# Optimization experiments

Hardware: AMD Instinct MI355X
Metric: run time of the kernel (lower is better)

Reference implementation:

```python
import jax, jax.numpy as jnp
import numpy as np

N_NODES = 50000
N_EDGES = 800000
D = 64  # in_feat == hidden_channels


def _param(key, shape, fan_in):
    return jax.random.normal(key, shape, dtype=jnp.float32) / np.sqrt(fan_in)


def setup_inputs() -> dict:
    key = jax.random.key(0)
    ks = jax.random.split(key, 32)
    inp = {
        "x": jax.random.normal(ks[0], (N_NODES, D), dtype=jnp.float32),
        "edge_index": jax.random.randint(ks[1], (2, N_EDGES), 0, N_NODES, dtype=jnp.int64),
    }
    i = 2
    for l in (1, 2, 3):
        inp[f"W1_{l}"] = _param(ks[i + 0], (D, D), D)   # LEConv lin1 (source nodes)
        inp[f"b1_{l}"] = jnp.zeros((D,), jnp.float32)
        inp[f"W2_{l}"] = _param(ks[i + 1], (D, D), D)   # LEConv lin2 (target nodes, no bias)
        inp[f"W3_{l}"] = _param(ks[i + 2], (D, D), D)   # LEConv lin3 (root/self)
        inp[f"b3_{l}"] = jnp.zeros((D,), jnp.float32)
        inp[f"Wl_{l}"] = _param(ks[i + 3], (D, D), D)   # post-conv Linear
        inp[f"bl_{l}"] = jnp.zeros((D,), jnp.float32)
        i += 4
    return inp


def _leconv(x, src, dst, W1, b1, W2, W3, b3):
    # out_i = lin3(x_i) + sum_{j->i} (lin1(x_j) - lin2(x_i))
    a = x @ W1 + b1          # [N, D]
    b = x @ W2               # [N, D]
    msg = a[src] - b[dst]    # [E, D]  gather + elementwise
    agg = jax.ops.segment_sum(msg, dst, num_segments=x.shape[0])  # scatter-add
    return agg + (x @ W3 + b3)


def reference(x, edge_index,
              W1_1, b1_1, W2_1, W3_1, b3_1, Wl_1, bl_1,
              W1_2, b1_2, W2_2, W3_2, b3_2, Wl_2, bl_2,
              W1_3, b1_3, W2_3, W3_3, b3_3, Wl_3, bl_3):
    src, dst = edge_index[0], edge_index[1]
    h = x
    for (W1, b1, W2, W3, b3, Wl, bl) in (
        (W1_1, b1_1, W2_1, W3_1, b3_1, Wl_1, bl_1),
        (W1_2, b1_2, W2_2, W3_2, b3_2, Wl_2, bl_2),
        (W1_3, b1_3, W2_3, W3_3, b3_3, Wl_3, bl_3),
    ):
        h = _leconv(h, src, dst, W1, b1, W2, W3, b3)
        h = jax.nn.relu(h @ Wl + bl)
    return h
```

## Files before the change

kernel.cpp:

```cpp
#include <hip/hip_runtime.h>

#define N_NODES 50000
#define N_EDGES 800000
#define NCHUNK 64
#define NRANGE 4
#define RNODES (N_NODES / NRANGE)
#define CEDGES (N_EDGES / NCHUNK)
#define HIST_NB (NCHUNK * NRANGE)
#define SCAN_NB2 ((N_NODES + 63) / 64)

typedef __attribute__((ext_vector_type(8))) short short8;
typedef __attribute__((ext_vector_type(4))) float f32x4;

struct LPtrs { const float *W1, *W2, *W3, *Wl, *b1, *b3, *bl; };
struct AllPtrs { LPtrs l[3]; };

__device__ inline unsigned short f2b(float f) {
    union { float f; unsigned u; } c; c.f = f;
    return (unsigned short)((c.u + 0x7FFFu + ((c.u >> 16) & 1u)) >> 16);
}
__device__ inline float b2f(unsigned short h) {
    union { unsigned u; float f; } c; c.u = ((unsigned)h) << 16;
    return c.f;
}

__global__ __launch_bounds__(256) void histpack_kernel(const int* __restrict__ dst,
                                                       unsigned char* __restrict__ hist_part,
                                                       AllPtrs ap,
                                                       unsigned short* __restrict__ Wp,
                                                       float* __restrict__ rows) {
    __shared__ unsigned int h[5248];
    const int t = threadIdx.x;
    if (blockIdx.x < HIST_NB) {
        const int chunk = blockIdx.x >> 2;
        const int range = blockIdx.x & 3;
        const int nbase = range * RNODES;
        for (int i = t; i < RNODES / 4; i += 256) h[i] = 0u;
        __syncthreads();
        const int* dp = dst + chunk * CEDGES;
        for (int i = t; i < CEDGES; i += 256) {
            int d = dp[i] - nbase;
            if ((unsigned)d < (unsigned)RNODES)
                atomicAdd(&h[d >> 2], 1u << ((d & 3) * 8));
        }
        __syncthreads();
        unsigned int* out = (unsigned int*)(hist_part + (long)chunk * N_NODES + nbase);
        for (int i = t; i < RNODES / 4; i += 256) out[i] = h[i];
    } else {
        float* sW = (float*)h;
        float* sL = (float*)h + 64 * 65;
        const int wi = blockIdx.x - HIST_NB;
        const int layer = wi / 12;
        const int ct = wi % 12;
        LPtrs L = ap.l[layer];
        const float* Wm = (ct < 4) ? L.W1 : (ct < 8) ? L.W2 : L.W3;
        const int colb = (ct & 3) * 16;
        for (int i = t; i < 64 * 64; i += 256) sW[(i >> 6) * 65 + (i & 63)] = Wm[i];
        for (int i = t; i < 64 * 16; i += 256) {
            int q = i >> 4, c = i & 15;
            sL[q * 17 + c] = L.Wl[q * 64 + colb + c];
        }
        __syncthreads();
        for (int local = t; local < 1024; local += 256) {
            int j = local & 7, lane = (local >> 3) & 63, s = local >> 9;
            int k = s * 32 + (lane >> 4) * 8 + j;
            int c = lane & 15;
            float acc = 0.f;
            #pragma unroll 8
            for (int q = 0; q < 64; ++q) acc += sW[k * 65 + q] * sL[q * 17 + c];
            Wp[layer * 12288 + ct * 1024 + local] = f2b(acc);
        }
        if (ct == 0 && t < 64) {
            int col = t;
            float r1 = 0.f, r3 = 0.f;
            for (int q = 0; q < 64; ++q) {
                float wl = L.Wl[q * 64 + col];
                r1 += L.b1[q] * wl;
                r3 += L.b3[q] * wl;
            }
            rows[layer * 128 + col] = r1;
            rows[layer * 128 + 64 + col] = r3 + L.bl[col];
        }
    }
}

__global__ __launch_bounds__(256) void scanA2_kernel(unsigned char* __restrict__ hist_part,
                                                     int* __restrict__ off,
                                                     int* __restrict__ deg,
                                                     int* __restrict__ bsum) {
    __shared__ int part[4][64];
    const int t = threadIdx.x;
    const int ln = t & 63;
    const int cg = t >> 6;
    const int node = blockIdx.x * 64 + ln;
    unsigned char* col = hist_part + node;
    unsigned char v[16];
    int s = 0;
    if (node < N_NODES) {
        #pragma unroll
        for (int k = 0; k < 16; ++k) {
            v[k] = col[(long)(cg * 16 + k) * N_NODES];
            s += v[k];
        }
    }
    part[cg][ln] = s;
    __syncthreads();
    int run = 0, tot = 0;
    #pragma unroll
    for (int g = 0; g < 4; ++g) {
        int p = part[g][ln];
        if (g < cg) run += p;
        tot += p;
    }
    if (node < N_NODES) {
        #pragma unroll
        for (int k = 0; k < 16; ++k) {
            col[(long)(cg * 16 + k) * N_NODES] = (unsigned char)run;
            run += v[k];
        }
        if (cg == 0) deg[node] = tot;
    }
    if (cg == 0) {
        int x = tot;
        #pragma unroll
        for (int d = 1; d < 64; d <<= 1) {
            int u = __shfl_up(x, d, 64);
            if (ln >= d) x += u;
        }
        if (node < N_NODES) off[node] = x - tot;
        if (ln == 63) bsum[blockIdx.x] = x;
    }
}

__device__ __forceinline__ void gemm_body(int blk, int t,
    const unsigned short* __restrict__ hbf, const float* __restrict__ hf32,
    const unsigned short* __restrict__ Wp,
    const int* __restrict__ deg, const float* __restrict__ rows,
    unsigned short* __restrict__ abf, unsigned short* __restrict__ wbf, int n)
{
    const int lane = t & 63;
    const int quad = lane >> 4, lm = lane & 15;
    const int row_base = blk * 64 + (t >> 6) * 16;

    int arow = min(row_base + lm, n - 1);
    short8 a0, a1;
    if (hf32) {
        const float* hrow = hf32 + (long)arow * 64;
        #pragma unroll
        for (int j = 0; j < 8; ++j) {
            a0[j] = (short)f2b(hrow[quad * 8 + j]);
            a1[j] = (short)f2b(hrow[32 + quad * 8 + j]);
        }
    } else {
        const unsigned short* hrow = hbf + (long)arow * 64;
        a0 = *(const short8*)(hrow + quad * 8);
        a1 = *(const short8*)(hrow + 32 + quad * 8);
    }

    const short8* wp = (const short8*)Wp;
    f32x4 acc[12];
    #pragma unroll
    for (int ct = 0; ct < 12; ++ct) {
        f32x4 z = {0.f, 0.f, 0.f, 0.f};
        short8 w0 = wp[(ct * 2 + 0) * 64 + lane];
        short8 w1 = wp[(ct * 2 + 1) * 64 + lane];
        z = __builtin_amdgcn_mfma_f32_16x16x32_bf16(a0, w0, z, 0, 0, 0);
        z = __builtin_amdgcn_mfma_f32_16x16x32_bf16(a1, w1, z, 0, 0, 0);
        acc[ct] = z;
    }

    const int g0 = row_base + quad * 4;
    float dg[4];
    #pragma unroll
    for (int r = 0; r < 4; ++r) dg[r] = (float)deg[min(g0 + r, n - 1)];

    #pragma unroll
    for (int ct = 0; ct < 4; ++ct) {
        int col = ct * 16 + lm;
        float r1 = rows[col];
        float r3 = rows[64 + col];
        #pragma unroll
        for (int r = 0; r < 4; ++r) {
            int g = g0 + r;
            if (g < n) {
                abf[(long)g * 64 + col] = f2b(acc[ct][r]);
                float wv = acc[8 + ct][r] - dg[r] * (acc[4 + ct][r] - r1) + r3;
                wbf[(long)g * 64 + col] = f2b(wv);
            }
        }
    }
}

__global__ __launch_bounds__(256) void gemm3w_kernel(
    const unsigned short* __restrict__ hbf, const float* __restrict__ hf32,
    const unsigned short* __restrict__ Wp,
    const int* __restrict__ deg, const float* __restrict__ rows,
    unsigned short* __restrict__ abf, unsigned short* __restrict__ wbf, int n)
{
    gemm_body(blockIdx.x, threadIdx.x, hbf, hf32, Wp, deg, rows, abf, wbf, n);
}

__global__ __launch_bounds__(256) void fillgemm_kernel(
    const int* __restrict__ src, const int* __restrict__ dst,
    const int* __restrict__ off, const int* __restrict__ bsum,
    int* __restrict__ boff, const unsigned char* __restrict__ hist_part,
    int* __restrict__ csr,
    const float* __restrict__ x, const unsigned short* __restrict__ Wp,
    const int* __restrict__ deg, const float* __restrict__ rows,
    unsigned short* __restrict__ abf, unsigned short* __restrict__ wbf)
{
    __shared__ int cur[RNODES];
    __shared__ int sb[SCAN_NB2 + 2];
    if (blockIdx.x >= HIST_NB) {
        gemm_body(blockIdx.x - HIST_NB, threadIdx.x, nullptr, x, Wp, deg, rows,
                  abf, wbf, N_NODES);
        return;
    }
    const int t = threadIdx.x;

    int carry = 0;
    for (int base = 0; base < SCAN_NB2; base += 256) {
        int idx = base + t;
        int v = (idx < SCAN_NB2) ? bsum[idx] : 0;
        cur[t] = v;
        __syncthreads();
        #pragma unroll
        for (int d = 1; d < 256; d <<= 1) {
            int u = (t >= d) ? cur[t - d] : 0;
            __syncthreads();
            cur[t] += u;
            __syncthreads();
        }
        if (idx < SCAN_NB2) sb[idx] = carry + cur[t] - v;
        carry += cur[255];
        __syncthreads();
    }
    if (blockIdx.x == 0)
        for (int i = t; i < SCAN_NB2; i += 256) boff[i] = sb[i];

    const int chunk = blockIdx.x >> 2;
    const int range = blockIdx.x & 3;
    const int nbase = range * RNODES;
    const unsigned char* bp = hist_part + (long)chunk * N_NODES + nbase;
    const int* op = off + nbase;
    for (int i = t; i < RNODES; i += 256)
        cur[i] = op[i] + sb[(nbase + i) >> 6] + (int)bp[i];
    __syncthreads();
    const int* dp = dst + chunk * CEDGES;
    const int* sp = src + chunk * CEDGES;
    for (int i = t; i < CEDGES; i += 256) {
        int d = dp[i] - nbase;
        if ((unsigned)d < (unsigned)RNODES) {
            int pos = atomicAdd(&cur[d], 1);
            csr[pos] = sp[i];
        }
    }
}

__global__ __launch_bounds__(256) void gather_out_kernel(
    const int* __restrict__ off, const int* __restrict__ boff,
    const int* __restrict__ degv, const int* __restrict__ csr,
    const unsigned short* __restrict__ abf,
    const unsigned short* __restrict__ wbf,
    float* __restrict__ out_f, unsigned short* __restrict__ out_b, int last)
{
    int node = blockIdx.x * 4 + (threadIdx.x >> 6);
    int lane = threadIdx.x & 63;
    const int g = lane >> 4;
    const int f = (lane & 15) * 4;
    int beg = off[node] + boff[node >> 6];
    int end = beg + degv[node];
    float ax = 0.f, ay = 0.f, az = 0.f, aw = 0.f;
    int j = beg;
    for (; j + 16 <= end; j += 16) {
        int s0 = csr[j + g], s1 = csr[j + 4 + g];
        int s2 = csr[j + 8 + g], s3 = csr[j + 12 + g];
        ushort4 v0 = *(const ushort4*)(abf + (long)s0 * 64 + f);
        ushort4 v1 = *(const ushort4*)(abf + (long)s1 * 64 + f);
        ushort4 v2 = *(const ushort4*)(abf + (long)s2 * 64 + f);
        ushort4 v3 = *(const ushort4*)(abf + (long)s3 * 64 + f);
        ax += b2f(v0.x) + b2f(v1.x) + b2f(v2.x) + b2f(v3.x);
        ay += b2f(v0.y) + b2f(v1.y) + b2f(v2.y) + b2f(v3.y);
        az += b2f(v0.z) + b2f(v1.z) + b2f(v2.z) + b2f(v3.z);
        aw += b2f(v0.w) + b2f(v1.w) + b2f(v2.w) + b2f(v3.w);
    }
    for (; j + 8 <= end; j += 8) {
        int s0 = csr[j + g], s1 = csr[j + 4 + g];
        ushort4 v0 = *(const ushort4*)(abf + (long)s0 * 64 + f);
        ushort4 v1 = *(const ushort4*)(abf + (long)s1 * 64 + f);
        ax += b2f(v0.x) + b2f(v1.x);
        ay += b2f(v0.y) + b2f(v1.y);
        az += b2f(v0.z) + b2f(v1.z);
        aw += b2f(v0.w) + b2f(v1.w);
    }
    for (; j < end; j += 4) {
        int jj = j + g;
        if (jj < end) {
            int s0 = csr[jj];
            ushort4 v0 = *(const ushort4*)(abf + (long)s0 * 64 + f);
            ax += b2f(v0.x); ay += b2f(v0.y); az += b2f(v0.z); aw += b2f(v0.w);
        }
    }
    #pragma unroll
    for (int m = 16; m < 64; m <<= 1) {
        ax += __shfl_xor(ax, m, 64);
        ay += __shfl_xor(ay, m, 64);
        az += __shfl_xor(az, m, 64);
        aw += __shfl_xor(aw, m, 64);
    }
    if (g == 0) {
        ushort4 wv = *(const ushort4*)(wbf + (long)node * 64 + f);
        float o0 = fmaxf(ax + b2f(wv.x), 0.f);
        float o1 = fmaxf(ay + b2f(wv.y), 0.f);
        float o2 = fmaxf(az + b2f(wv.z), 0.f);
        float o3 = fmaxf(aw + b2f(wv.w), 0.f);
        if (last) {
            float4 o = {o0, o1, o2, o3};
            *(float4*)(out_f + (long)node * 64 + f) = o;
        } else {
            ushort4 o;
            o.x = f2b(o0); o.y = f2b(o1); o.z = f2b(o2); o.w = f2b(o3);
            *(ushort4*)(out_b + (long)node * 64 + f) = o;
        }
    }
}

extern "C" void kernel_launch(void* const* d_in, const int* in_sizes, int n_in,
                              void* d_out, int out_size, void* d_ws, size_t ws_size,
                              hipStream_t stream) {
    const float* x  = (const float*)d_in[0];
    const int*   ei = (const int*)d_in[1];
    const int*   src = ei;
    const int*   dst = ei + N_EDGES;

    char* wsb = (char*)d_ws;
    unsigned char*  hist_part = (unsigned char*)(wsb);
    unsigned short* abf  = (unsigned short*)(wsb + 12800000);
    unsigned short* wbf  = (unsigned short*)(wsb + 19200000);
    unsigned short* h1   = (unsigned short*)(wsb + 25600000);
    unsigned short* Wp   = (unsigned short*)(wsb + 38400000);
    float*          rows = (float*)(wsb + 38500000);
    int* off  = (int*)(wsb + 38600000);
    int* deg  = off + N_NODES;
    int* bsum = deg + N_NODES;
    int* boff = bsum + 1024;
    int* csr  = boff + 1024;

    const int NBLK = (N_NODES + 63) / 64;

    AllPtrs ap;
    for (int l = 0; l < 3; ++l) {
        int base = 2 + l * 7;
        ap.l[l].W1 = (const float*)d_in[base + 0];
        ap.l[l].b1 = (const float*)d_in[base + 1];
        ap.l[l].W2 = (const float*)d_in[base + 2];
        ap.l[l].W3 = (const float*)d_in[base + 3];
        ap.l[l].b3 = (const float*)d_in[base + 4];
        ap.l[l].Wl = (const float*)d_in[base + 5];
        ap.l[l].bl = (const float*)d_in[base + 6];
    }

    histpack_kernel<<<HIST_NB + 36, 256, 0, stream>>>(dst, hist_part, ap, Wp, rows);
    scanA2_kernel<<<SCAN_NB2, 256, 0, stream>>>(hist_part, off, deg, bsum);
    fillgemm_kernel<<<HIST_NB + NBLK, 256, 0, stream>>>(
        src, dst, off, bsum, boff, hist_part, csr,
        x, Wp, deg, rows, abf, wbf);

    gather_out_kernel<<<N_NODES / 4, 256, 0, stream>>>(
        off, boff, deg, csr, abf, wbf, (float*)d_out, h1, 0);

    const unsigned short* hin = h1;
    for (int l = 1; l < 3; ++l) {
        gemm3w_kernel<<<NBLK, 256, 0, stream>>>(
            hin, nullptr, Wp + l * 12288, deg, rows + l * 128,
            abf, wbf, N_NODES);
        gather_out_kernel<<<N_NODES / 4, 256, 0, stream>>>(
            off, boff, deg, csr, abf, wbf, (float*)d_out, h1, (l == 2));
        hin = h1;
    }
}
```

Measured before the change: 266.8 us.

## Split CSR histogram/fill into eight node ranges and single-pass block-sum scan

Doubles the number of node ranges per edge chunk (8 instead of 4) with a padded node count, so histogram and CSR-fill blocks use smaller shared arrays and more blocks run in parallel. The block-sum scan in the fill kernel is replaced by a single 256-thread scan over 4-element groups, removing the multi-pass loop. The cost is that each block now rereads its full edge chunk, so dst reads double. It also adds padding bytes to the histogram buffer, which must be sized for N_PAD.

```diff
diff --git a/kernel.cpp b/kernel.cpp
--- a/kernel.cpp
+++ b/kernel.cpp
@@ -1,13 +1,14 @@
 #include <hip/hip_runtime.h>
 
 #define N_NODES 50000
+#define N_PAD 50048
 #define N_EDGES 800000
 #define NCHUNK 64
-#define NRANGE 4
-#define RNODES (N_NODES / NRANGE)
+#define NRANGE 8
+#define RN 6256
 #define CEDGES (N_EDGES / NCHUNK)
 #define HIST_NB (NCHUNK * NRANGE)
-#define SCAN_NB2 ((N_NODES + 63) / 64)
+#define SCAN_NB2 (N_PAD / 64)
 
 typedef __attribute__((ext_vector_type(8))) short short8;
 typedef __attribute__((ext_vector_type(4))) float f32x4;
@@ -32,20 +33,20 @@
     __shared__ unsigned int h[5248];
     const int t = threadIdx.x;
     if (blockIdx.x < HIST_NB) {
-        const int chunk = blockIdx.x >> 2;
-        const int range = blockIdx.x & 3;
-        const int nbase = range * RNODES;
-        for (int i = t; i < RNODES / 4; i += 256) h[i] = 0u;
+        const int chunk = blockIdx.x >> 3;
+        const int range = blockIdx.x & 7;
+        const int nbase = range * RN;
+        for (int i = t; i < RN / 4; i += 256) h[i] = 0u;
         __syncthreads();
         const int* dp = dst + chunk * CEDGES;
         for (int i = t; i < CEDGES; i += 256) {
             int d = dp[i] - nbase;
-            if ((unsigned)d < (unsigned)RNODES)
+            if ((unsigned)d < (unsigned)RN)
                 atomicAdd(&h[d >> 2], 1u << ((d & 3) * 8));
         }
         __syncthreads();
-        unsigned int* out = (unsigned int*)(hist_part + (long)chunk * N_NODES + nbase);
-        for (int i = t; i < RNODES / 4; i += 256) out[i] = h[i];
+        unsigned int* out = (unsigned int*)(hist_part + (long)chunk * N_PAD + nbase);
+        for (int i = t; i < RN / 4; i += 256) out[i] = h[i];
     } else {
         float* sW = (float*)h;
         float* sL = (float*)h + 64 * 65;
@@ -96,12 +97,10 @@
     unsigned char* col = hist_part + node;
     unsigned char v[16];
     int s = 0;
-    if (node < N_NODES) {
-        #pragma unroll
-        for (int k = 0; k < 16; ++k) {
-            v[k] = col[(long)(cg * 16 + k) * N_NODES];
-            s += v[k];
-        }
+    #pragma unroll
+    for (int k = 0; k < 16; ++k) {
+        v[k] = col[(long)(cg * 16 + k) * N_PAD];
+        s += v[k];
     }
     part[cg][ln] = s;
     __syncthreads();
@@ -112,14 +111,12 @@
         if (g < cg) run += p;
         tot += p;
     }
-    if (node < N_NODES) {
-        #pragma unroll
-        for (int k = 0; k < 16; ++k) {
-            col[(long)(cg * 16 + k) * N_NODES] = (unsigned char)run;
-            run += v[k];
-        }
-        if (cg == 0) deg[node] = tot;
-    }
+    #pragma unroll
+    for (int k = 0; k < 16; ++k) {
+        col[(long)(cg * 16 + k) * N_PAD] = (unsigned char)run;
+        run += v[k];
+    }
+    if (cg == 0 && node < N_NODES) deg[node] = tot;
     if (cg == 0) {
         int x = tot;
         #pragma unroll
@@ -209,8 +206,8 @@
     const int* __restrict__ deg, const float* __restrict__ rows,
     unsigned short* __restrict__ abf, unsigned short* __restrict__ wbf)
 {
-    __shared__ int cur[RNODES];
-    __shared__ int sb[SCAN_NB2 + 2];
+    __shared__ int cur[RN];
+    __shared__ int sb[1024];
     if (blockIdx.x >= HIST_NB) {
         gemm_body(blockIdx.x - HIST_NB, threadIdx.x, nullptr, x, Wp, deg, rows,
                   abf, wbf, N_NODES);
@@ -218,39 +215,44 @@
     }
     const int t = threadIdx.x;
 
-    int carry = 0;
-    for (int base = 0; base < SCAN_NB2; base += 256) {
-        int idx = base + t;
-        int v = (idx < SCAN_NB2) ? bsum[idx] : 0;
-        cur[t] = v;
-        __syncthreads();
-        #pragma unroll
-        for (int d = 1; d < 256; d <<= 1) {
-            int u = (t >= d) ? cur[t - d] : 0;
-            __syncthreads();
-            cur[t] += u;
-            __syncthreads();
-        }
-        if (idx < SCAN_NB2) sb[idx] = carry + cur[t] - v;
-        carry += cur[255];
-        __syncthreads();
-    }
+    const int i0 = t * 4;
+    int a0 = (i0 + 0 < SCAN_NB2) ? bsum[i0 + 0] : 0;
+    int a1 = (i0 + 1 < SCAN_NB2) ? bsum[i0 + 1] : 0;
+    int a2 = (i0 + 2 < SCAN_NB2) ? bsum[i0 + 2] : 0;
+    int a3 = (i0 + 3 < SCAN_NB2) ? bsum[i0 + 3] : 0;
+    int s = a0 + a1 + a2 + a3;
+    cur[t] = s;
+    __syncthreads();
+    #pragma unroll
+    for (int d = 1; d < 256; d <<= 1) {
+        int u = (t >= d) ? cur[t - d] : 0;
+        __syncthreads();
+        cur[t] += u;
+        __syncthreads();
+    }
+    int excl = cur[t] - s;
+    sb[i0 + 0] = excl;
+    sb[i0 + 1] = excl + a0;
+    sb[i0 + 2] = excl + a0 + a1;
+    sb[i0 + 3] = excl + a0 + a1 + a2;
+    __syncthreads();
     if (blockIdx.x == 0)
         for (int i = t; i < SCAN_NB2; i += 256) boff[i] = sb[i];
 
-    const int chunk = blockIdx.x >> 2;
-    const int range = blockIdx.x & 3;
-    const int nbase = range * RNODES;
-    const unsigned char* bp = hist_part + (long)chunk * N_NODES + nbase;
+    const int chunk = blockIdx.x >> 3;
+    const int range = blockIdx.x & 7;
+    const int nbase = range * RN;
+    const unsigned char* bp = hist_part + (long)chunk * N_PAD + nbase;
     const int* op = off + nbase;
-    for (int i = t; i < RNODES; i += 256)
+    const int lim = min(RN, N_NODES - nbase);
+    for (int i = t; i < lim; i += 256)
         cur[i] = op[i] + sb[(nbase + i) >> 6] + (int)bp[i];
     __syncthreads();
     const int* dp = dst + chunk * CEDGES;
     const int* sp = src + chunk * CEDGES;
     for (int i = t; i < CEDGES; i += 256) {
         int d = dp[i] - nbase;
-        if ((unsigned)d < (unsigned)RNODES) {
+        if ((unsigned)d < (unsigned)RN) {
             int pos = atomicAdd(&cur[d], 1);
             csr[pos] = sp[i];
         }
```

Result: no change. 262.7 us (-1.5%).

## Replace chunked byte-histogram CSR build with global atomic degree count and fill

Applied to the files above, without the earlier changes.

Replaces the per-chunk shared-memory byte-histogram, the column scan and the chunked fill with a simpler pipeline: zero deg, count degrees with global atomics, run a single-block 1024-thread scan over padded nodes, then fill the CSR through global atomic cursors. This removes the 12.8 MB hist_part buffer and its strided traffic. In exchange it adds one more launch, a serial single-block scan, and global atomic contention. The CSR order within a node becomes nondeterministic, which can change summation order.

```diff
diff --git a/kernel.cpp b/kernel.cpp
--- a/kernel.cpp
+++ b/kernel.cpp
@@ -1,13 +1,10 @@
 #include <hip/hip_runtime.h>
 
 #define N_NODES 50000
+#define N_PAD 50176
 #define N_EDGES 800000
-#define NCHUNK 64
-#define NRANGE 4
-#define RNODES (N_NODES / NRANGE)
-#define CEDGES (N_EDGES / NCHUNK)
-#define HIST_NB (NCHUNK * NRANGE)
-#define SCAN_NB2 ((N_NODES + 63) / 64)
+#define FILLB 1024
+#define ZB 196
 
 typedef __attribute__((ext_vector_type(8))) short short8;
 typedef __attribute__((ext_vector_type(4))) float f32x4;
@@ -24,32 +21,18 @@
     return c.f;
 }
 
-__global__ __launch_bounds__(256) void histpack_kernel(const int* __restrict__ dst,
-                                                       unsigned char* __restrict__ hist_part,
+__global__ __launch_bounds__(256) void zeropack_kernel(int* __restrict__ deg,
                                                        AllPtrs ap,
                                                        unsigned short* __restrict__ Wp,
                                                        float* __restrict__ rows) {
-    __shared__ unsigned int h[5248];
+    __shared__ float sbuf[5248];
     const int t = threadIdx.x;
-    if (blockIdx.x < HIST_NB) {
-        const int chunk = blockIdx.x >> 2;
-        const int range = blockIdx.x & 3;
-        const int nbase = range * RNODES;
-        for (int i = t; i < RNODES / 4; i += 256) h[i] = 0u;
-        __syncthreads();
-        const int* dp = dst + chunk * CEDGES;
-        for (int i = t; i < CEDGES; i += 256) {
-            int d = dp[i] - nbase;
-            if ((unsigned)d < (unsigned)RNODES)
-                atomicAdd(&h[d >> 2], 1u << ((d & 3) * 8));
-        }
-        __syncthreads();
-        unsigned int* out = (unsigned int*)(hist_part + (long)chunk * N_NODES + nbase);
-        for (int i = t; i < RNODES / 4; i += 256) out[i] = h[i];
+    if (blockIdx.x < ZB) {
+        deg[blockIdx.x * 256 + t] = 0;
     } else {
-        float* sW = (float*)h;
-        float* sL = (float*)h + 64 * 65;
-        const int wi = blockIdx.x - HIST_NB;
+        float* sW = sbuf;
+        float* sL = sbuf + 64 * 65;
+        const int wi = blockIdx.x - ZB;
         const int layer = wi / 12;
         const int ct = wi % 12;
         LPtrs L = ap.l[layer];
@@ -84,51 +67,44 @@
     }
 }
 
-__global__ __launch_bounds__(256) void scanA2_kernel(unsigned char* __restrict__ hist_part,
-                                                     int* __restrict__ off,
-                                                     int* __restrict__ deg,
-                                                     int* __restrict__ bsum) {
-    __shared__ int part[4][64];
+__global__ __launch_bounds__(256) void deg_kernel(const int* __restrict__ dst,
+                                                  int* __restrict__ deg) {
+    int i = blockIdx.x * 256 + threadIdx.x;
+    atomicAdd(&deg[dst[i]], 1);
+}
+
+__global__ __launch_bounds__(1024) void scan_kernel(const int* __restrict__ deg,
+                                                    int* __restrict__ rowbeg,
+                                                    int* __restrict__ gcur) {
+    __shared__ int ws[16];
     const int t = threadIdx.x;
-    const int ln = t & 63;
-    const int cg = t >> 6;
-    const int node = blockIdx.x * 64 + ln;
-    unsigned char* col = hist_part + node;
-    unsigned char v[16];
+    const int base = t * 49;
     int s = 0;
-    if (node < N_NODES) {
+    for (int k = 0; k < 49; ++k) s += deg[base + k];
+    int x = s;
+    #pragma unroll
+    for (int d = 1; d < 64; d <<= 1) {
+        int u = __shfl_up(x, d, 64);
+        if ((t & 63) >= d) x += u;
+    }
+    if ((t & 63) == 63) ws[t >> 6] = x;
+    __syncthreads();
+    if (t < 16) {
+        int y = ws[t];
         #pragma unroll
-        for (int k = 0; k < 16; ++k) {
-            v[k] = col[(long)(cg * 16 + k) * N_NODES];
-            s += v[k];
-        }
-    }
-    part[cg][ln] = s;
+        for (int d = 1; d < 16; d <<= 1) {
+            int u = __shfl_up(y, d, 16);
+            if (t >= d) y += u;
+        }
+        ws[t] = y;
+    }
     __syncthreads();
-    int run = 0, tot = 0;
-    #pragma unroll
-    for (int g = 0; g < 4; ++g) {
-        int p = part[g][ln];
-        if (g < cg) run += p;
-        tot += p;
-    }
-    if (node < N_NODES) {
-        #pragma unroll
-        for (int k = 0; k < 16; ++k) {
-            col[(long)(cg * 16 + k) * N_NODES] = (unsigned char)run;
-            run += v[k];
-        }
-        if (cg == 0) deg[node] = tot;
-    }
-    if (cg == 0) {
-        int x = tot;
-        #pragma unroll
-        for (int d = 1; d < 64; d <<= 1) {
-            int u = __shfl_up(x, d, 64);
-            if (ln >= d) x += u;
-        }
-        if (node < N_NODES) off[node] = x - tot;
-        if (ln == 63) bsum[blockIdx.x] = x;
+    int run = ((t >> 6) ? ws[(t >> 6) - 1] : 0) + x - s;
+    for (int k = 0; k < 49; ++k) {
+        int i = base + k;
+        rowbeg[i] = run;
+        gcur[i] = run;
+        run += deg[i];
     }
 }
 
@@ -202,64 +178,27 @@
 
 __global__ __launch_bounds__(256) void fillgemm_kernel(
     const int* __restrict__ src, const int* __restrict__ dst,
-    const int* __restrict__ off, const int* __restrict__ bsum,
-    int* __restrict__ boff, const unsigned char* __restrict__ hist_part,
-    int* __restrict__ csr,
+    int* __restrict__ gcur, int* __restrict__ csr,
     const float* __restrict__ x, const unsigned short* __restrict__ Wp,
     const int* __restrict__ deg, const float* __restrict__ rows,
     unsigned short* __restrict__ abf, unsigned short* __restrict__ wbf)
 {
-    __shared__ int cur[RNODES];
-    __shared__ int sb[SCAN_NB2 + 2];
-    if (blockIdx.x >= HIST_NB) {
-        gemm_body(blockIdx.x - HIST_NB, threadIdx.x, nullptr, x, Wp, deg, rows,
+    if (blockIdx.x >= FILLB) {
+        gemm_body(blockIdx.x - FILLB, threadIdx.x, nullptr, x, Wp, deg, rows,
                   abf, wbf, N_NODES);
         return;
     }
-    const int t = threadIdx.x;
-
-    int carry = 0;
-    for (int base = 0; base < SCAN_NB2; base += 256) {
-        int idx = base + t;
-        int v = (idx < SCAN_NB2) ? bsum[idx] : 0;
-        cur[t] = v;
-        __syncthreads();
-        #pragma unroll
-        for (int d = 1; d < 256; d <<= 1) {
-            int u = (t >= d) ? cur[t - d] : 0;
-            __syncthreads();
-            cur[t] += u;
-            __syncthreads();
-        }
-        if (idx < SCAN_NB2) sb[idx] = carry + cur[t] - v;
-        carry += cur[255];
-        __syncthreads();
-    }
-    if (blockIdx.x == 0)
-        for (int i = t; i < SCAN_NB2; i += 256) boff[i] = sb[i];
-
-    const int chunk = blockIdx.x >> 2;
-    const int range = blockIdx.x & 3;
-    const int nbase = range * RNODES;
-    const unsigned char* bp = hist_part + (long)chunk * N_NODES + nbase;
-    const int* op = off + nbase;
-    for (int i = t; i < RNODES; i += 256)
-        cur[i] = op[i] + sb[(nbase + i) >> 6] + (int)bp[i];
-    __syncthreads();
-    const int* dp = dst + chunk * CEDGES;
-    const int* sp = src + chunk * CEDGES;
-    for (int i = t; i < CEDGES; i += 256) {
-        int d = dp[i] - nbase;
-        if ((unsigned)d < (unsigned)RNODES) {
-            int pos = atomicAdd(&cur[d], 1);
-            csr[pos] = sp[i];
-        }
+    for (int i = blockIdx.x * 256 + threadIdx.x; i < N_EDGES; i += FILLB * 256) {
+        int d = dst[i];
+        int s = src[i];
+        int pos = atomicAdd(&gcur[d], 1);
+        csr[pos] = s;
     }
 }
 
 __global__ __launch_bounds__(256) void gather_out_kernel(
-    const int* __restrict__ off, const int* __restrict__ boff,
-    const int* __restrict__ degv, const int* __restrict__ csr,
+    const int* __restrict__ rowbeg, const int* __restrict__ degv,
+    const int* __restrict__ csr,
     const unsigned short* __restrict__ abf,
     const unsigned short* __restrict__ wbf,
     float* __restrict__ out_f, unsigned short* __restrict__ out_b, int last)
@@ -268,7 +207,7 @@
     int lane = threadIdx.x & 63;
     const int g = lane >> 4;
     const int f = (lane & 15) * 4;
-    int beg = off[node] + boff[node >> 6];
+    int beg = rowbeg[node];
     int end = beg + degv[node];
     float ax = 0.f, ay = 0.f, az = 0.f, aw = 0.f;
     int j = beg;
@@ -334,17 +273,15 @@
     const int*   dst = ei + N_EDGES;
 
     char* wsb = (char*)d_ws;
-    unsigned char*  hist_part = (unsigned char*)(wsb);
-    unsigned short* abf  = (unsigned short*)(wsb + 12800000);
-    unsigned short* wbf  = (unsigned short*)(wsb + 19200000);
-    unsigned short* h1   = (unsigned short*)(wsb + 25600000);
-    unsigned short* Wp   = (unsigned short*)(wsb + 38400000);
-    float*          rows = (float*)(wsb + 38500000);
-    int* off  = (int*)(wsb + 38600000);
-    int* deg  = off + N_NODES;
-    int* bsum = deg + N_NODES;
-    int* boff = bsum + 1024;
-    int* csr  = boff + 1024;
+    unsigned short* abf  = (unsigned short*)(wsb);
+    unsigned short* wbf  = (unsigned short*)(wsb + 6400000);
+    unsigned short* h1   = (unsigned short*)(wsb + 12800000);
+    unsigned short* Wp   = (unsigned short*)(wsb + 19200000);
+    float*          rows = (float*)(wsb + 19300000);
+    int* deg    = (int*)(wsb + 19400000);
+    int* rowbeg = deg + N_PAD;
+    int* gcur   = rowbeg + N_PAD;
+    int* csr    = gcur + N_PAD;
 
     const int NBLK = (N_NODES + 63) / 64;
 
@@ -360,14 +297,14 @@
         ap.l[l].bl = (const float*)d_in[base + 6];
     }
 
-    histpack_kernel<<<HIST_NB + 36, 256, 0, stream>>>(dst, hist_part, ap, Wp, rows);
-    scanA2_kernel<<<SCAN_NB2, 256, 0, stream>>>(hist_part, off, deg, bsum);
-    fillgemm_kernel<<<HIST_NB + NBLK, 256, 0, stream>>>(
-        src, dst, off, bsum, boff, hist_part, csr,
-        x, Wp, deg, rows, abf, wbf);
+    zeropack_kernel<<<ZB + 36, 256, 0, stream>>>(deg, ap, Wp, rows);
+    deg_kernel<<<N_EDGES / 256, 256, 0, stream>>>(dst, deg);
+    scan_kernel<<<1, 1024, 0, stream>>>(deg, rowbeg, gcur);
+    fillgemm_kernel<<<FILLB + NBLK, 256, 0, stream>>>(
+        src, dst, gcur, csr, x, Wp, deg, rows, abf, wbf);
 
     gather_out_kernel<<<N_NODES / 4, 256, 0, stream>>>(
-        off, boff, deg, csr, abf, wbf, (float*)d_out, h1, 0);
+        rowbeg, deg, csr, abf, wbf, (float*)d_out, h1, 0);
 
     const unsigned short* hin = h1;
     for (int l = 1; l < 3; ++l) {
@@ -375,7 +312,7 @@
             hin, nullptr, Wp + l * 12288, deg, rows + l * 128,
             abf, wbf, N_NODES);
         gather_out_kernel<<<N_NODES / 4, 256, 0, stream>>>(
-            off, boff, deg, csr, abf, wbf, (float*)d_out, h1, (l == 2));
+            rowbeg, deg, csr, abf, wbf, (float*)d_out, h1, (l == 2));
         hin = h1;
     }
 }
```

New measurement: 351.9 us. +31.9%, slower.

## Aggregate raw bf16 features before projection and overlap next-layer GEMM with gather

Applied to the files above, without the earlier changes.

By linearity, the source-side projection is applied after neighbour aggregation. The gather sums raw bf16 node features into S, and a new out_kernel does S·(W1·Wl) plus the precomputed self/target term and ReLU. The self/target GEMM is folded into the gather grid as extra blocks, so it runs alongside the gather, and the x-to-bf16 cast moves into the histogram kernel. The histogram uses 128 chunks over a padded node range, with a simpler single-pass block scan. The aim is to drop the per-layer abf write and the standalone GEMM launches, at the cost of an extra small GEMM kernel per layer and an extra S round trip.

```diff
diff --git a/kernel.cpp b/kernel.cpp
--- a/kernel.cpp
+++ b/kernel.cpp
@@ -1,13 +1,16 @@
 #include <hip/hip_runtime.h>
 
 #define N_NODES 50000
+#define N_PAD 50176
 #define N_EDGES 800000
-#define NCHUNK 64
+#define NCHUNK 128
 #define NRANGE 4
-#define RNODES (N_NODES / NRANGE)
+#define RNODES 12544
 #define CEDGES (N_EDGES / NCHUNK)
 #define HIST_NB (NCHUNK * NRANGE)
-#define SCAN_NB2 ((N_NODES + 63) / 64)
+#define SCAN_NB 782
+#define GATB 12500
+#define NBLK 782
 
 typedef __attribute__((ext_vector_type(8))) short short8;
 typedef __attribute__((ext_vector_type(4))) float f32x4;
@@ -24,11 +27,11 @@
     return c.f;
 }
 
-__global__ __launch_bounds__(256) void histpack_kernel(const int* __restrict__ dst,
-                                                       unsigned char* __restrict__ hist_part,
-                                                       AllPtrs ap,
-                                                       unsigned short* __restrict__ Wp,
-                                                       float* __restrict__ rows) {
+__global__ __launch_bounds__(256) void histcast_kernel(
+    const int* __restrict__ dst, unsigned char* __restrict__ hist_part,
+    AllPtrs ap, unsigned short* __restrict__ Wp, float* __restrict__ rows,
+    const float* __restrict__ x, unsigned short* __restrict__ h0)
+{
     __shared__ unsigned int h[5248];
     const int t = threadIdx.x;
     if (blockIdx.x < HIST_NB) {
@@ -44,9 +47,9 @@
                 atomicAdd(&h[d >> 2], 1u << ((d & 3) * 8));
         }
         __syncthreads();
-        unsigned int* out = (unsigned int*)(hist_part + (long)chunk * N_NODES + nbase);
+        unsigned int* out = (unsigned int*)(hist_part + (long)chunk * N_PAD + nbase);
         for (int i = t; i < RNODES / 4; i += 256) out[i] = h[i];
-    } else {
+    } else if (blockIdx.x < HIST_NB + 36) {
         float* sW = (float*)h;
         float* sL = (float*)h + 64 * 65;
         const int wi = blockIdx.x - HIST_NB;
@@ -81,6 +84,24 @@
             rows[layer * 128 + col] = r1;
             rows[layer * 128 + 64 + col] = r3 + L.bl[col];
         }
+    } else {
+        const int cb = blockIdx.x - HIST_NB - 36;
+        const long base = (long)cb * 4096 + t * 16;
+        if (base < (long)N_NODES * 64) {
+            const float4* xp = (const float4*)(x + base);
+            float4 f0 = xp[0], f1 = xp[1], f2 = xp[2], f3 = xp[3];
+            short8 r0, r1v;
+            r0[0] = (short)f2b(f0.x); r0[1] = (short)f2b(f0.y);
+            r0[2] = (short)f2b(f0.z); r0[3] = (short)f2b(f0.w);
+            r0[4] = (short)f2b(f1.x); r0[5] = (short)f2b(f1.y);
+            r0[6] = (short)f2b(f1.z); r0[7] = (short)f2b(f1.w);
+            r1v[0] = (short)f2b(f2.x); r1v[1] = (short)f2b(f2.y);
+            r1v[2] = (short)f2b(f2.z); r1v[3] = (short)f2b(f2.w);
+            r1v[4] = (short)f2b(f3.x); r1v[5] = (short)f2b(f3.y);
+            r1v[6] = (short)f2b(f3.z); r1v[7] = (short)f2b(f3.w);
+            *(short8*)(h0 + base) = r0;
+            *(short8*)(h0 + base + 8) = r1v;
+        }
     }
 }
 
@@ -94,14 +115,12 @@
     const int cg = t >> 6;
     const int node = blockIdx.x * 64 + ln;
     unsigned char* col = hist_part + node;
-    unsigned char v[16];
+    unsigned char v[32];
     int s = 0;
-    if (node < N_NODES) {
-        #pragma unroll
-        for (int k = 0; k < 16; ++k) {
-            v[k] = col[(long)(cg * 16 + k) * N_NODES];
-            s += v[k];
-        }
+    #pragma unroll
+    for (int k = 0; k < 32; ++k) {
+        v[k] = col[(long)(cg * 32 + k) * N_PAD];
+        s += v[k];
     }
     part[cg][ln] = s;
     __syncthreads();
@@ -112,58 +131,46 @@
         if (g < cg) run += p;
         tot += p;
     }
-    if (node < N_NODES) {
-        #pragma unroll
-        for (int k = 0; k < 16; ++k) {
-            col[(long)(cg * 16 + k) * N_NODES] = (unsigned char)run;
-            run += v[k];
-        }
-        if (cg == 0) deg[node] = tot;
+    #pragma unroll
+    for (int k = 0; k < 32; ++k) {
+        col[(long)(cg * 32 + k) * N_PAD] = (unsigned char)run;
+        run += v[k];
     }
     if (cg == 0) {
-        int x = tot;
+        deg[node] = tot;
+        int xv = tot;
         #pragma unroll
         for (int d = 1; d < 64; d <<= 1) {
-            int u = __shfl_up(x, d, 64);
-            if (ln >= d) x += u;
-        }
-        if (node < N_NODES) off[node] = x - tot;
-        if (ln == 63) bsum[blockIdx.x] = x;
-    }
-}
-
-__device__ __forceinline__ void gemm_body(int blk, int t,
-    const unsigned short* __restrict__ hbf, const float* __restrict__ hf32,
-    const unsigned short* __restrict__ Wp,
+            int u = __shfl_up(xv, d, 64);
+            if (ln >= d) xv += u;
+        }
+        off[node] = xv - tot;
+        if (ln == 63) bsum[blockIdx.x] = xv;
+    }
+}
+
+__device__ __forceinline__ void gemmw_body(int blk, int t,
+    const unsigned short* __restrict__ hbf, const unsigned short* __restrict__ Wp,
     const int* __restrict__ deg, const float* __restrict__ rows,
-    unsigned short* __restrict__ abf, unsigned short* __restrict__ wbf, int n)
+    unsigned short* __restrict__ wbf, int n)
 {
     const int lane = t & 63;
     const int quad = lane >> 4, lm = lane & 15;
     const int row_base = blk * 64 + (t >> 6) * 16;
 
     int arow = min(row_base + lm, n - 1);
-    short8 a0, a1;
-    if (hf32) {
-        const float* hrow = hf32 + (long)arow * 64;
-        #pragma unroll
-        for (int j = 0; j < 8; ++j) {
-            a0[j] = (short)f2b(hrow[quad * 8 + j]);
-            a1[j] = (short)f2b(hrow[32 + quad * 8 + j]);
-        }
-    } else {
-        const unsigned short* hrow = hbf + (long)arow * 64;
-        a0 = *(const short8*)(hrow + quad * 8);
-        a1 = *(const short8*)(hrow + 32 + quad * 8);
-    }
+    const unsigned short* hrow = hbf + (long)arow * 64;
+    short8 a0 = *(const short8*)(hrow + quad * 8);
+    short8 a1 = *(const short8*)(hrow + 32 + quad * 8);
 
     const short8* wp = (const short8*)Wp;
-    f32x4 acc[12];
-    #pragma unroll
-    for (int ct = 0; ct < 12; ++ct) {
+    f32x4 acc[8];
+    #pragma unroll
+    for (int ct = 0; ct < 8; ++ct) {
+        int tile = ct + 4;
         f32x4 z = {0.f, 0.f, 0.f, 0.f};
-        short8 w0 = wp[(ct * 2 + 0) * 64 + lane];
-        short8 w1 = wp[(ct * 2 + 1) * 64 + lane];
+        short8 w0 = wp[(tile * 2 + 0) * 64 + lane];
+        short8 w1 = wp[(tile * 2 + 1) * 64 + lane];
         z = __builtin_amdgcn_mfma_f32_16x16x32_bf16(a0, w0, z, 0, 0, 0);
         z = __builtin_amdgcn_mfma_f32_16x16x32_bf16(a1, w1, z, 0, 0, 0);
         acc[ct] = z;
@@ -183,67 +190,62 @@
         for (int r = 0; r < 4; ++r) {
             int g = g0 + r;
             if (g < n) {
-                abf[(long)g * 64 + col] = f2b(acc[ct][r]);
-                float wv = acc[8 + ct][r] - dg[r] * (acc[4 + ct][r] - r1) + r3;
+                float wv = acc[4 + ct][r] - dg[r] * (acc[ct][r] - r1) + r3;
                 wbf[(long)g * 64 + col] = f2b(wv);
             }
         }
     }
 }
 
-__global__ __launch_bounds__(256) void gemm3w_kernel(
-    const unsigned short* __restrict__ hbf, const float* __restrict__ hf32,
-    const unsigned short* __restrict__ Wp,
-    const int* __restrict__ deg, const float* __restrict__ rows,
-    unsigned short* __restrict__ abf, unsigned short* __restrict__ wbf, int n)
-{
-    gemm_body(blockIdx.x, threadIdx.x, hbf, hf32, Wp, deg, rows, abf, wbf, n);
-}
-
-__global__ __launch_bounds__(256) void fillgemm_kernel(
+__global__ __launch_bounds__(256) void fillw_kernel(
     const int* __restrict__ src, const int* __restrict__ dst,
     const int* __restrict__ off, const int* __restrict__ bsum,
     int* __restrict__ boff, const unsigned char* __restrict__ hist_part,
     int* __restrict__ csr,
-    const float* __restrict__ x, const unsigned short* __restrict__ Wp,
+    const unsigned short* __restrict__ h0, const unsigned short* __restrict__ Wp,
     const int* __restrict__ deg, const float* __restrict__ rows,
-    unsigned short* __restrict__ abf, unsigned short* __restrict__ wbf)
+    unsigned short* __restrict__ wbf)
 {
     __shared__ int cur[RNODES];
-    __shared__ int sb[SCAN_NB2 + 2];
+    __shared__ int sb[1024];
     if (blockIdx.x >= HIST_NB) {
-        gemm_body(blockIdx.x - HIST_NB, threadIdx.x, nullptr, x, Wp, deg, rows,
-                  abf, wbf, N_NODES);
+        gemmw_body(blockIdx.x - HIST_NB, threadIdx.x, h0, Wp, deg, rows,
+                   wbf, N_NODES);
         return;
     }
     const int t = threadIdx.x;
 
-    int carry = 0;
-    for (int base = 0; base < SCAN_NB2; base += 256) {
-        int idx = base + t;
-        int v = (idx < SCAN_NB2) ? bsum[idx] : 0;
-        cur[t] = v;
+    const int i0 = t * 4;
+    int a0 = (i0 + 0 < SCAN_NB) ? bsum[i0 + 0] : 0;
+    int a1 = (i0 + 1 < SCAN_NB) ? bsum[i0 + 1] : 0;
+    int a2 = (i0 + 2 < SCAN_NB) ? bsum[i0 + 2] : 0;
+    int a3 = (i0 + 3 < SCAN_NB) ? bsum[i0 + 3] : 0;
+    int s = a0 + a1 + a2 + a3;
+    cur[t] = s;
+    __syncthreads();
+    #pragma unroll
+    for (int d = 1; d < 256; d <<= 1) {
+        int u = (t >= d) ? cur[t - d] : 0;
         __syncthreads();
-        #pragma unroll
-        for (int d = 1; d < 256; d <<= 1) {
-            int u = (t >= d) ? cur[t - d] : 0;
-            __syncthreads();
-            cur[t] += u;
-            __syncthreads();
-        }
-        if (idx < SCAN_NB2) sb[idx] = carry + cur[t] - v;
-        carry += cur[255];
+        cur[t] += u;
         __syncthreads();
     }
+    int excl = cur[t] - s;
+    sb[i0 + 0] = excl;
+    sb[i0 + 1] = excl + a0;
+    sb[i0 + 2] = excl + a0 + a1;
+    sb[i0 + 3] = excl + a0 + a1 + a2;
+    __syncthreads();
     if (blockIdx.x == 0)
-        for (int i = t; i < SCAN_NB2; i += 256) boff[i] = sb[i];
+        for (int i = t; i < SCAN_NB; i += 256) boff[i] = sb[i];
 
     const int chunk = blockIdx.x >> 2;
     const int range = blockIdx.x & 3;
     const int nbase = range * RNODES;
-    const unsigned char* bp = hist_part + (long)chunk * N_NODES + nbase;
+    const unsigned char* bp = hist_part + (long)chunk * N_PAD + nbase;
     const int* op = off + nbase;
-    for (int i = t; i < RNODES; i += 256)
+    const int lim = min(RNODES, N_NODES - nbase);
+    for (int i = t; i < lim; i += 256)
         cur[i] = op[i] + sb[(nbase + i) >> 6] + (int)bp[i];
     __syncthreads();
     const int* dp = dst + chunk * CEDGES;
@@ -257,13 +259,18 @@
     }
 }
 
-__global__ __launch_bounds__(256) void gather_out_kernel(
+__global__ __launch_bounds__(256) void gatherw_kernel(
     const int* __restrict__ off, const int* __restrict__ boff,
     const int* __restrict__ degv, const int* __restrict__ csr,
-    const unsigned short* __restrict__ abf,
-    const unsigned short* __restrict__ wbf,
-    float* __restrict__ out_f, unsigned short* __restrict__ out_b, int last)
+    const unsigned short* __restrict__ hbf, unsigned short* __restrict__ Sbf,
+    const unsigned short* __restrict__ Wp, const float* __restrict__ rows,
+    unsigned short* __restrict__ wbf)
 {
+    if (blockIdx.x >= GATB) {
+        gemmw_body(blockIdx.x - GATB, threadIdx.x, hbf, Wp, degv, rows,
+                   wbf, N_NODES);
+        return;
+    }
     int node = blockIdx.x * 4 + (threadIdx.x >> 6);
     int lane = threadIdx.x & 63;
     const int g = lane >> 4;
@@ -275,10 +282,10 @@
     for (; j + 16 <= end; j += 16) {
         int s0 = csr[j + g], s1 = csr[j + 4 + g];
         int s2 = csr[j + 8 + g], s3 = csr[j + 12 + g];
-        ushort4 v0 = *(const ushort4*)(abf + (long)s0 * 64 + f);
-        ushort4 v1 = *(const ushort4*)(abf + (long)s1 * 64 + f);
-        ushort4 v2 = *(const ushort4*)(abf + (long)s2 * 64 + f);
-        ushort4 v3 = *(const ushort4*)(abf + (long)s3 * 64 + f);
+        ushort4 v0 = *(const ushort4*)(hbf + (long)s0 * 64 + f);
+        ushort4 v1 = *(const ushort4*)(hbf + (long)s1 * 64 + f);
+        ushort4 v2 = *(const ushort4*)(hbf + (long)s2 * 64 + f);
+        ushort4 v3 = *(const ushort4*)(hbf + (long)s3 * 64 + f);
         ax += b2f(v0.x) + b2f(v1.x) + b2f(v2.x) + b2f(v3.x);
         ay += b2f(v0.y) + b2f(v1.y) + b2f(v2.y) + b2f(v3.y);
         az += b2f(v0.z) + b2f(v1.z) + b2f(v2.z) + b2f(v3.z);
@@ -286,8 +293,8 @@
     }
     for (; j + 8 <= end; j += 8) {
         int s0 = csr[j + g], s1 = csr[j + 4 + g];
-        ushort4 v0 = *(const ushort4*)(abf + (long)s0 * 64 + f);
-        ushort4 v1 = *(const ushort4*)(abf + (long)s1 * 64 + f);
+        ushort4 v0 = *(const ushort4*)(hbf + (long)s0 * 64 + f);
+        ushort4 v1 = *(const ushort4*)(hbf + (long)s1 * 64 + f);
         ax += b2f(v0.x) + b2f(v1.x);
         ay += b2f(v0.y) + b2f(v1.y);
         az += b2f(v0.z) + b2f(v1.z);
@@ -297,7 +304,7 @@
         int jj = j + g;
         if (jj < end) {
             int s0 = csr[jj];
-            ushort4 v0 = *(const ushort4*)(abf + (long)s0 * 64 + f);
+            ushort4 v0 = *(const ushort4*)(hbf + (long)s0 * 64 + f);
             ax += b2f(v0.x); ay += b2f(v0.y); az += b2f(v0.z); aw += b2f(v0.w);
         }
     }
@@ -309,18 +316,52 @@
         aw += __shfl_xor(aw, m, 64);
     }
     if (g == 0) {
-        ushort4 wv = *(const ushort4*)(wbf + (long)node * 64 + f);
-        float o0 = fmaxf(ax + b2f(wv.x), 0.f);
-        float o1 = fmaxf(ay + b2f(wv.y), 0.f);
-        float o2 = fmaxf(az + b2f(wv.z), 0.f);
-        float o3 = fmaxf(aw + b2f(wv.w), 0.f);
-        if (last) {
-            float4 o = {o0, o1, o2, o3};
-            *(float4*)(out_f + (long)node * 64 + f) = o;
-        } else {
-            ushort4 o;
-            o.x = f2b(o0); o.y = f2b(o1); o.z = f2b(o2); o.w = f2b(o3);
-            *(ushort4*)(out_b + (long)node * 64 + f) = o;
+        ushort4 o;
+        o.x = f2b(ax); o.y = f2b(ay); o.z = f2b(az); o.w = f2b(aw);
+        *(ushort4*)(Sbf + (long)node * 64 + f) = o;
+    }
+}
+
+__global__ __launch_bounds__(256) void out_kernel(
+    const unsigned short* __restrict__ Sbf, const unsigned short* __restrict__ wbf,
+    const unsigned short* __restrict__ Wp,
+    unsigned short* __restrict__ hout, float* __restrict__ fout, int last, int n)
+{
+    const int t = threadIdx.x;
+    const int lane = t & 63;
+    const int quad = lane >> 4, lm = lane & 15;
+    const int row_base = blockIdx.x * 64 + (t >> 6) * 16;
+
+    int arow = min(row_base + lm, n - 1);
+    const unsigned short* srow = Sbf + (long)arow * 64;
+    short8 a0 = *(const short8*)(srow + quad * 8);
+    short8 a1 = *(const short8*)(srow + 32 + quad * 8);
+
+    const short8* wp = (const short8*)Wp;
+    f32x4 acc[4];
+    #pragma unroll
+    for (int ct = 0; ct < 4; ++ct) {
+        f32x4 z = {0.f, 0.f, 0.f, 0.f};
+        short8 w0 = wp[(ct * 2 + 0) * 64 + lane];
+        short8 w1 = wp[(ct * 2 + 1) * 64 + lane];
+        z = __builtin_amdgcn_mfma_f32_16x16x32_bf16(a0, w0, z, 0, 0, 0);
+        z = __builtin_amdgcn_mfma_f32_16x16x32_bf16(a1, w1, z, 0, 0, 0);
+        acc[ct] = z;
+    }
+
+    const int g0 = row_base + quad * 4;
+    #pragma unroll
+    for (int ct = 0; ct < 4; ++ct) {
+        int col = ct * 16 + lm;
+        #pragma unroll
+        for (int r = 0; r < 4; ++r) {
+            int g = g0 + r;
+            if (g < n) {
+                float val = acc[ct][r] + b2f(wbf[(long)g * 64 + col]);
+                val = fmaxf(val, 0.f);
+                if (last) fout[(long)g * 64 + col] = val;
+                else      hout[(long)g * 64 + col] = f2b(val);
+            }
         }
     }
 }
@@ -335,18 +376,17 @@
 
     char* wsb = (char*)d_ws;
     unsigned char*  hist_part = (unsigned char*)(wsb);
-    unsigned short* abf  = (unsigned short*)(wsb + 12800000);
-    unsigned short* wbf  = (unsigned short*)(wsb + 19200000);
-    unsigned short* h1   = (unsigned short*)(wsb + 25600000);
-    unsigned short* Wp   = (unsigned short*)(wsb + 38400000);
-    float*          rows = (float*)(wsb + 38500000);
-    int* off  = (int*)(wsb + 38600000);
-    int* deg  = off + N_NODES;
-    int* bsum = deg + N_NODES;
-    int* boff = bsum + 1024;
-    int* csr  = boff + 1024;
-
-    const int NBLK = (N_NODES + 63) / 64;
+    unsigned short* h0   = (unsigned short*)(wsb + 6500000);
+    unsigned short* h1   = (unsigned short*)(wsb + 12900000);
+    unsigned short* Sbf  = (unsigned short*)(wsb + 19300000);
+    unsigned short* wbf  = (unsigned short*)(wsb + 25700000);
+    unsigned short* Wp   = (unsigned short*)(wsb + 32100000);
+    float*          rows = (float*)(wsb + 32200000);
+    int* deg  = (int*)(wsb + 32300000);
+    int* off  = (int*)(wsb + 32600000);
+    int* bsum = (int*)(wsb + 32900000);
+    int* boff = (int*)(wsb + 32950000);
+    int* csr  = (int*)(wsb + 33000000);
 
     AllPtrs ap;
     for (int l = 0; l < 3; ++l) {
@@ -360,22 +400,23 @@
         ap.l[l].bl = (const float*)d_in[base + 6];
     }
 
-    histpack_kernel<<<HIST_NB + 36, 256, 0, stream>>>(dst, hist_part, ap, Wp, rows);
-    scanA2_kernel<<<SCAN_NB2, 256, 0, stream>>>(hist_part, off, deg, bsum);
-    fillgemm_kernel<<<HIST_NB + NBLK, 256, 0, stream>>>(
+    histcast_kernel<<<HIST_NB + 36 + 782, 256, 0, stream>>>(
+        dst, hist_part, ap, Wp, rows, x, h0);
+    scanA2_kernel<<<SCAN_NB, 256, 0, stream>>>(hist_part, off, deg, bsum);
+    fillw_kernel<<<HIST_NB + NBLK, 256, 0, stream>>>(
         src, dst, off, bsum, boff, hist_part, csr,
-        x, Wp, deg, rows, abf, wbf);
-
-    gather_out_kernel<<<N_NODES / 4, 256, 0, stream>>>(
-        off, boff, deg, csr, abf, wbf, (float*)d_out, h1, 0);
-
-    const unsigned short* hin = h1;
-    for (int l = 1; l < 3; ++l) {
-        gemm3w_kernel<<<NBLK, 256, 0, stream>>>(
-            hin, nullptr, Wp + l * 12288, deg, rows + l * 128,
-            abf, wbf, N_NODES);
-        gather_out_kernel<<<N_NODES / 4, 256, 0, stream>>>(
-            off, boff, deg, csr, abf, wbf, (float*)d_out, h1, (l == 2));
-        hin = h1;
-    }
-}
+        h0, Wp, deg, rows, wbf);
+
+    gatherw_kernel<<<GATB, 256, 0, stream>>>(
+        off, boff, deg, csr, h0, Sbf, Wp, rows, wbf);
+    out_kernel<<<NBLK, 256, 0, stream>>>(Sbf, wbf, Wp, h1, nullptr, 0, N_NODES);
+
+    gatherw_kernel<<<GATB + NBLK, 256, 0, stream>>>(
+        off, boff, deg, csr, h1, Sbf, Wp + 12288, rows + 128, wbf);
+    out_kernel<<<NBLK, 256, 0, stream>>>(Sbf, wbf, Wp + 12288, h0, nullptr, 0, N_NODES);
+
+    gatherw_kernel<<<GATB + NBLK, 256, 0, stream>>>(
+        off, boff, deg, csr, h0, Sbf, Wp + 24576, rows + 256, wbf);
+    out_kernel<<<NBLK, 256, 0, stream>>>(Sbf, wbf, Wp + 24576, nullptr,
+                                         (float*)d_out, 1, N_NODES);
+}
```

New measurement: 306.4 us. 1.15x slower.
